# Kernel tuning notes

Hardware: AMD Instinct MI355X
Metric: run time of the kernel (lower is better)

Reference implementation:

```python
import jax, jax.numpy as jnp
import numpy as np

LEVEL_SHAPES = [(100, 134), (50, 67), (25, 34), (13, 17)]  # (H, W) per feature level
NH, NL, NP, D, DFF = 8, 4, 4, 256, 1024
DH = D // NH
LTOT = sum(h * w for h, w in LEVEL_SHAPES)  # 17821
BS, NQ = 4, 300


def _ln(x, w, b):
    m = x.mean(-1, keepdims=True)
    v = ((x - m) ** 2).mean(-1, keepdims=True)
    return (x - m) / jnp.sqrt(v + 1e-5) * w + b


def _mha(q, k, v, in_w, in_b, out_w, out_b):
    B, N, _ = q.shape
    wq, wk, wv = jnp.split(in_w, 3, axis=0)
    bq, bk, bv = jnp.split(in_b, 3)
    qh = (q @ wq.T + bq).reshape(B, N, NH, DH)
    kh = (k @ wk.T + bk).reshape(B, N, NH, DH)
    vh = (v @ wv.T + bv).reshape(B, N, NH, DH)
    a = jax.nn.softmax(jnp.einsum('bqhd,bkhd->bhqk', qh, kh) / float(np.sqrt(DH)), axis=-1)
    o = jnp.einsum('bhqk,bkhd->bqhd', a, vh).reshape(B, N, D)
    return o @ out_w.T + out_b


def _bilinear(img, grid):
    # img [B,C,H,W]; grid [B,N,2] in [-1,1]; align_corners=False, zero padding
    B, C, H, W = img.shape
    x = (grid[..., 0] + 1.0) * 0.5 * W - 0.5
    y = (grid[..., 1] + 1.0) * 0.5 * H - 0.5
    x0f = jnp.floor(x); y0f = jnp.floor(y)
    wx = x - x0f; wy = y - y0f
    x0 = x0f.astype(jnp.int32); y0 = y0f.astype(jnp.int32)
    flat = img.reshape(B, C, H * W)

    def gather(xi, yi):
        m = ((xi >= 0) & (xi < W) & (yi >= 0) & (yi < H)).astype(img.dtype)
        idx = jnp.clip(yi, 0, H - 1) * W + jnp.clip(xi, 0, W - 1)
        g = jnp.take_along_axis(flat, jnp.broadcast_to(idx[:, None, :], (B, C, idx.shape[-1])), axis=2)
        return g * m[:, None, :]

    return (gather(x0, y0) * ((1 - wx) * (1 - wy))[:, None]
            + gather(x0 + 1, y0) * (wx * (1 - wy))[:, None]
            + gather(x0, y0 + 1) * ((1 - wx) * wy)[:, None]
            + gather(x0 + 1, y0 + 1) * (wx * wy)[:, None])


def _msdeform(value, loc, aw):
    # value [B,L,NH,DH]; loc [B,Nq,NH,NL,NP,2] in [0,1]; aw [B,Nq,NH,NL,NP]
    B, Nq = loc.shape[0], loc.shape[1]
    outs = []
    start = 0
    for l, (Hl, Wl) in enumerate(LEVEL_SHAPES):
        v = value[:, start:start + Hl * Wl].transpose(0, 2, 3, 1).reshape(B * NH, DH, Hl, Wl)
        g = (2.0 * loc[:, :, :, l] - 1.0).transpose(0, 2, 1, 3, 4).reshape(B * NH, Nq * NP, 2)
        outs.append(_bilinear(v, g).reshape(B * NH, DH, Nq, NP))
        start += Hl * Wl
    samp = jnp.stack(outs, axis=3)  # [B*NH, DH, Nq, NL, NP]
    w = aw.transpose(0, 2, 1, 3, 4).reshape(B * NH, 1, Nq, NL, NP)
    out = (samp * w).sum(axis=(3, 4))  # [B*NH, DH, Nq]
    return out.reshape(B, NH, DH, Nq).transpose(0, 3, 1, 2).reshape(B, Nq, D)


def _deform_branch(q, ref, src_other, vw, vb, ow, ob, aww, awb, outw, outb):
    B, Nq, _ = q.shape
    value = (src_other @ vw.T + vb).reshape(B, -1, NH, DH)
    off = (q @ ow.T + ob).reshape(B, Nq, NH, NL, NP, 2)
    aw = jax.nn.softmax((q @ aww.T + awb).reshape(B, Nq, NH, NL * NP), axis=-1).reshape(B, Nq, NH, NL, NP)
    norm = jnp.array([[w, h] for h, w in LEVEL_SHAPES], dtype=q.dtype)  # (W,H) per level
    loc = ref[:, :, None, :, None, :] + off / norm[None, None, None, :, None, :]
    return _msdeform(value, loc, aw) @ outw.T + outb


def reference(tgt_RGB, tgt_T, query_pos_RGB, query_pos_T, ref_RGB, ref_T, src_RGB, src_T,
              sa_in_w, sa_in_b, sa_out_w, sa_out_b, ln_w, ln_b,
              ffn_w1, ffn_b1, ffn_w2, ffn_b2,
              val_w, val_b, off_w, off_b, aw_w, aw_b, cout_w, cout_b):
    # --- dual self-attention (eval mode: dropout = identity) ---
    q_RGB = tgt_RGB + query_pos_RGB
    q_T = tgt_T + query_pos_T
    sa_RGB = _mha(q_RGB, q_RGB, tgt_RGB, sa_in_w[0], sa_in_b[0], sa_out_w[0], sa_out_b[0])
    sa_T = _mha(q_T, q_T, tgt_T, sa_in_w[1], sa_in_b[1], sa_out_w[1], sa_out_b[1])
    tgt_RGB = _ln(tgt_RGB + sa_RGB, ln_w[0, 1], ln_b[0, 1])  # norm2_RGB
    tgt_T = _ln(tgt_T + sa_T, ln_w[1, 1], ln_b[1, 1])        # norm2_T
    # --- interactive multi-scale deformable cross-attn: RGB queries sample T memory & vice versa ---
    qc_RGB = tgt_RGB + query_pos_RGB
    qc_T = tgt_T + query_pos_T
    t2_RGB = _deform_branch(qc_RGB, ref_RGB, src_T, val_w[0], val_b[0], off_w[0], off_b[0], aw_w[0], aw_b[0], cout_w[0], cout_b[0])
    t2_T = _deform_branch(qc_T, ref_T, src_RGB, val_w[1], val_b[1], off_w[1], off_b[1], aw_w[1], aw_b[1], cout_w[1], cout_b[1])
    F_RGB, F_T = t2_RGB, t2_T
    # cross residuals exactly as in the torch layer (note the modality swap)
    r = tgt_T + t2_RGB
    t = r + t2_T
    tgt_RGB = _ln(r, ln_w[0, 0], ln_b[0, 0])  # norm1_RGB
    tgt_T = _ln(t, ln_w[1, 0], ln_b[1, 0])    # norm1_T
    # --- FFNs ---
    tgt_RGB = _ln(tgt_RGB + (jax.nn.relu(tgt_RGB @ ffn_w1[0].T + ffn_b1[0]) @ ffn_w2[0].T + ffn_b2[0]), ln_w[0, 2], ln_b[0, 2])
    tgt_T = _ln(tgt_T + (jax.nn.relu(tgt_T @ ffn_w1[1].T + ffn_b1[1]) @ ffn_w2[1].T + ffn_b2[1]), ln_w[1, 2], ln_b[1, 2])
    return tgt_RGB, tgt_T, F_RGB, F_T


def setup_inputs() -> dict:
    key = jax.random.key(0)
    ks = jax.random.split(key, 24)
    s = 0.05
    w = lambda k, shp: jax.random.normal(k, shp, dtype=jnp.float32) * s
    return {
        'tgt_RGB': jax.random.normal(ks[0], (BS, NQ, D), jnp.float32),
        'tgt_T': jax.random.normal(ks[1], (BS, NQ, D), jnp.float32),
        'query_pos_RGB': jax.random.normal(ks[2], (BS, NQ, D), jnp.float32),
        'query_pos_T': jax.random.normal(ks[3], (BS, NQ, D), jnp.float32),
        'ref_RGB': jax.random.uniform(ks[4], (BS, NQ, NL, 2), jnp.float32),
        'ref_T': jax.random.uniform(ks[5], (BS, NQ, NL, 2), jnp.float32),
        'src_RGB': jax.random.normal(ks[6], (BS, LTOT, D), jnp.float32),
        'src_T': jax.random.normal(ks[7], (BS, LTOT, D), jnp.float32),
        'sa_in_w': w(ks[8], (2, 3 * D, D)),
        'sa_in_b': jnp.zeros((2, 3 * D), jnp.float32),
        'sa_out_w': w(ks[9], (2, D, D)),
        'sa_out_b': jnp.zeros((2, D), jnp.float32),
        'ln_w': jnp.ones((2, 3, D), jnp.float32),
        'ln_b': jnp.zeros((2, 3, D), jnp.float32),
        'ffn_w1': w(ks[10], (2, DFF, D)),
        'ffn_b1': jnp.zeros((2, DFF), jnp.float32),
        'ffn_w2': w(ks[11], (2, D, DFF)),
        'ffn_b2': jnp.zeros((2, D), jnp.float32),
        'val_w': w(ks[12], (2, D, D)),
        'val_b': jnp.zeros((2, D), jnp.float32),
        'off_w': w(ks[13], (2, NH * NL * NP * 2, D)),
        'off_b': jax.random.normal(ks[14], (2, NH * NL * NP * 2), jnp.float32) * 0.5,
        'aw_w': w(ks[15], (2, NH * NL * NP, D)),
        'aw_b': jnp.zeros((2, NH * NL * NP), jnp.float32),
        'cout_w': w(ks[16], (2, D, D)),
        'cout_b': jnp.zeros((2, D), jnp.float32),
    }
```

## Files before the change

### kernel.cpp

```cpp
#include <hip/hip_runtime.h>
#include <hip/hip_bf16.h>
#include <cstddef>
#include <math.h>

#define NTOK 1200
#define LTOT_C 17821
#define MVAL 71284
#define STOK (NTOK * 256)

typedef __attribute__((ext_vector_type(8))) short bhalf8;
typedef __attribute__((ext_vector_type(4))) float f32x4;

static __device__ __forceinline__ short f2bf(float f) {
    unsigned u = __builtin_bit_cast(unsigned, f);
    u += 0x7fffu + ((u >> 16) & 1u);
    return (short)(u >> 16);
}
static __device__ __forceinline__ float bf2f(short s) {
    unsigned u = ((unsigned)(unsigned short)s) << 16;
    return __builtin_bit_cast(float, u);
}
static __device__ __forceinline__ bhalf8 cvt8(float4 a, float4 b) {
    bhalf8 h;
    h[0] = f2bf(a.x); h[1] = f2bf(a.y); h[2] = f2bf(a.z); h[3] = f2bf(a.w);
    h[4] = f2bf(b.x); h[5] = f2bf(b.y); h[6] = f2bf(b.z); h[7] = f2bf(b.w);
    return h;
}
static __device__ __forceinline__ void gload_lds16(const void* g, void* l) {
    __builtin_amdgcn_global_load_lds(
        (const __attribute__((address_space(1))) void*)g,
        (__attribute__((address_space(3))) void*)l, 16, 0, 0);
}

struct WcvtArgs { const float* s[10]; short* d[10]; int n[10]; };
__global__ __launch_bounds__(256) void wcvt(WcvtArgs a) {
    const int ti = blockIdx.y;
    const float* s = a.s[ti];
    short* d = a.d[ti];
    const int n = a.n[ti];
    for (int base = (blockIdx.x * 256 + threadIdx.x) * 8; base < n; base += gridDim.x * 256 * 8) {
        const float4 f0 = *reinterpret_cast<const float4*>(s + base);
        const float4 f1 = *reinterpret_cast<const float4*>(s + base + 4);
        *reinterpret_cast<bhalf8*>(d + base) = cvt8(f0, f1);
    }
}

__global__ __launch_bounds__(256) void prep_act(
    const float* __restrict__ tgt0, const float* __restrict__ tgt1,
    const float* __restrict__ pos0, const float* __restrict__ pos1,
    short* __restrict__ qb_bf, short* __restrict__ tgtb,
    const float* __restrict__ off_b, const float* __restrict__ aw_b,
    float* __restrict__ baw)
{
    const int z = blockIdx.y;
    if (blockIdx.x == 0 && z == 0) {
        for (int i = threadIdx.x; i < 768; i += 256) {
            const int zz = i / 384, j = i - zz * 384;
            baw[i] = (j < 256) ? off_b[zz * 256 + j] : aw_b[zz * 128 + (j - 256)];
        }
    }
    const float* tg = z ? tgt1 : tgt0;
    const float* ps = z ? pos1 : pos0;
    const int base = (blockIdx.x * 256 + threadIdx.x) * 8;
    if (base >= STOK) return;
    const float4 t0 = *reinterpret_cast<const float4*>(tg + base);
    const float4 t1 = *reinterpret_cast<const float4*>(tg + base + 4);
    const float4 p0 = *reinterpret_cast<const float4*>(ps + base);
    const float4 p1 = *reinterpret_cast<const float4*>(ps + base + 4);
    float4 s0 = make_float4(t0.x + p0.x, t0.y + p0.y, t0.z + p0.z, t0.w + p0.w);
    float4 s1 = make_float4(t1.x + p1.x, t1.y + p1.y, t1.z + p1.z, t1.w + p1.w);
    *reinterpret_cast<bhalf8*>(qb_bf + (size_t)z * STOK + base) = cvt8(s0, s1);
    *reinterpret_cast<bhalf8*>(tgtb + (size_t)z * STOK + base) = cvt8(t0, t1);
}

__global__ __launch_bounds__(256) void gemm_val(
    const float* __restrict__ A0, const float* __restrict__ A1,
    const short* __restrict__ Wbf, const float* __restrict__ bias,
    short* __restrict__ C)
{
    __shared__ alignas(16) short As[2][64 * 64];
    __shared__ alignas(16) short Bs[2][128 * 64];
    const int i = blockIdx.x;
    const int widx = (i & 7) * 557 + (i >> 3);
    const int x = widx & 1;
    const int yz = widx >> 1;
    const int z = yz / 1114;
    const int y = yz - z * 1114;
    const float* A = z ? A1 : A0;
    const short* W = Wbf + (size_t)z * 65536;
    const float* bz = bias + z * 256;
    short* Cz = C + (size_t)z * MVAL * 256;
    const int t = threadIdx.x;
    const int wave = t >> 6, lane = t & 63;
    const int l15 = lane & 15, l4 = lane >> 4;
    const int wr = wave >> 1, wc = wave & 1;
    const int bm = y * 64, bn = x * 128;
    f32x4 acc[2][4] = {};

    const int nr8 = lane >> 3, q8 = lane & 7;
    auto stageW = [&](int k0, int buf) {
        #pragma unroll
        for (int ii = 0; ii < 4; ++ii) {
            const int c = wave * 4 + ii;
            const int n = c * 8 + nr8;
            gload_lds16(W + (size_t)(bn + n) * 256 + k0 + ((q8 ^ nr8) << 3),
                        (char*)&Bs[buf][0] + c * 1024);
        }
    };
    float4 paf[2][2];
    auto issueA = [&](int k0) {
        #pragma unroll
        for (int ii = 0; ii < 2; ++ii) {
            const int G = t + ii * 256;
            const int m = G >> 3, g = G & 7;
            const int row = min(bm + m, MVAL - 1);
            const float* s = A + (size_t)row * 256 + k0 + g * 8;
            paf[ii][0] = *reinterpret_cast<const float4*>(s);
            paf[ii][1] = *reinterpret_cast<const float4*>(s + 4);
        }
    };
    auto commitA = [&](int buf) {
        #pragma unroll
        for (int ii = 0; ii < 2; ++ii) {
            const int G = t + ii * 256;
            const int m = G >> 3, g = G & 7;
            *reinterpret_cast<bhalf8*>(&As[buf][m * 64 + ((g ^ (m & 7)) << 3)]) =
                cvt8(paf[ii][0], paf[ii][1]);
        }
    };
    auto compute = [&](int buf) {
        #pragma unroll
        for (int kf = 0; kf < 2; ++kf) {
            bhalf8 af[2], bfv[4];
            #pragma unroll
            for (int mf = 0; mf < 2; ++mf) {
                const int m = wr * 32 + (mf << 4) + l15;
                const int g = ((kf << 2) + l4) ^ (m & 7);
                af[mf] = *reinterpret_cast<const bhalf8*>(&As[buf][m * 64 + (g << 3)]);
            }
            #pragma unroll
            for (int nf = 0; nf < 4; ++nf) {
                const int n = (wc << 6) + (nf << 4) + l15;
                const int g = ((kf << 2) + l4) ^ (n & 7);
                bfv[nf] = *reinterpret_cast<const bhalf8*>(&Bs[buf][n * 64 + (g << 3)]);
            }
            #pragma unroll
            for (int mf = 0; mf < 2; ++mf)
                #pragma unroll
                for (int nf = 0; nf < 4; ++nf)
                    acc[mf][nf] = __builtin_amdgcn_mfma_f32_16x16x32_bf16(
                        af[mf], bfv[nf], acc[mf][nf], 0, 0, 0);
        }
    };

    issueA(0);
    stageW(0, 0);
    commitA(0);
    __syncthreads();
    #pragma unroll
    for (int ks = 0; ks < 4; ++ks) {
        const int cur = ks & 1, nxt = cur ^ 1;
        if (ks + 1 < 4) {
            issueA((ks + 1) << 6);
            stageW((ks + 1) << 6, nxt);
        }
        compute(cur);
        if (ks + 1 < 4) commitA(nxt);
        __syncthreads();
    }

    float br[4];
    #pragma unroll
    for (int nf = 0; nf < 4; ++nf) br[nf] = bz[bn + (wc << 6) + (nf << 4) + l15];
    #pragma unroll
    for (int mf = 0; mf < 2; ++mf) {
        #pragma unroll
        for (int j = 0; j < 4; ++j) {
            const int row = bm + wr * 32 + (mf << 4) + (l4 << 2) + j;
            if (row >= MVAL) continue;
            const int colbase = bn + (wc << 6);
            #pragma unroll
            for (int nf = 0; nf < 4; ++nf)
                Cz[(size_t)row * 256 + colbase + (nf << 4) + l15] = f2bf(acc[mf][nf][j] + br[nf]);
        }
    }
}

template<bool HASRES, bool RELU, bool OUT_BF16, int BM, int NK>
__global__ __launch_bounds__(256) void gemm_bf16(
    const short* __restrict__ Av, size_t aStrideZ, int lda,
    const short* __restrict__ Wv, size_t wStrideZ, int ldw,
    const float* __restrict__ bias, size_t biasStrideZ,
    const float* __restrict__ Res0, const float* __restrict__ Res1, int ldr,
    void* __restrict__ Cv, size_t cStrideZ, int ldc,
    int M)
{
    constexpr int MFR = BM / 32;
    constexpr int ACW = BM / 32;
    __shared__ alignas(16) short As[2][BM * 64];
    __shared__ alignas(16) short Bs[2][128 * 64];
    const int z = blockIdx.z;
    const short* W = Wv + (size_t)z * wStrideZ;
    const float* bz = bias + (size_t)z * biasStrideZ;
    const int t = threadIdx.x;
    const int wave = t >> 6, lane = t & 63;
    const int l15 = lane & 15, l4 = lane >> 4;
    const int wr = wave >> 1, wc = wave & 1;
    const int bm = blockIdx.y * BM, bn = blockIdx.x * 128;
    f32x4 acc[MFR][4] = {};

    const int nr8 = lane >> 3, q8 = lane & 7;
    auto stageW = [&](int k0, int buf) {
        #pragma unroll
        for (int i = 0; i < 4; ++i) {
            const int c = wave * 4 + i;
            const int n = c * 8 + nr8;
            gload_lds16(W + (size_t)(bn + n) * ldw + k0 + ((q8 ^ nr8) << 3),
                        (char*)&Bs[buf][0] + c * 1024);
        }
    };
    auto stageA = [&](int k0, int buf) {
        #pragma unroll
        for (int i = 0; i < ACW; ++i) {
            const int c = wave * ACW + i;
            const int m = c * 8 + nr8;
            const int row = min(bm + m, M - 1);
            gload_lds16(Av + (size_t)z * aStrideZ + (size_t)row * lda + k0 + ((q8 ^ (m & 7)) << 3),
                        (char*)&As[buf][0] + c * 1024);
        }
    };
    auto compute = [&](int buf) {
        #pragma unroll
        for (int kf = 0; kf < 2; ++kf) {
            bhalf8 af[MFR], bfv[4];
            #pragma unroll
            for (int mf = 0; mf < MFR; ++mf) {
                const int m = wr * (BM / 2) + (mf << 4) + l15;
                const int g = ((kf << 2) + l4) ^ (m & 7);
                af[mf] = *reinterpret_cast<const bhalf8*>(&As[buf][m * 64 + (g << 3)]);
            }
            #pragma unroll
            for (int nf = 0; nf < 4; ++nf) {
                const int n = (wc << 6) + (nf << 4) + l15;
                const int g = ((kf << 2) + l4) ^ (n & 7);
                bfv[nf] = *reinterpret_cast<const bhalf8*>(&Bs[buf][n * 64 + (g << 3)]);
            }
            #pragma unroll
            for (int mf = 0; mf < MFR; ++mf)
                #pragma unroll
                for (int nf = 0; nf < 4; ++nf)
                    acc[mf][nf] = __builtin_amdgcn_mfma_f32_16x16x32_bf16(
                        af[mf], bfv[nf], acc[mf][nf], 0, 0, 0);
        }
    };

    stageA(0, 0);
    stageW(0, 0);
    __syncthreads();
    #pragma unroll
    for (int ks = 0; ks < NK; ++ks) {
        const int cur = ks & 1, nxt = cur ^ 1;
        if (ks + 1 < NK) {
            stageA((ks + 1) << 6, nxt);
            stageW((ks + 1) << 6, nxt);
        }
        compute(cur);
        __syncthreads();
    }

    const float* Rz = HASRES ? (z ? Res1 : Res0) : nullptr;
    float br[4];
    #pragma unroll
    for (int nf = 0; nf < 4; ++nf) br[nf] = bz[bn + (wc << 6) + (nf << 4) + l15];
    #pragma unroll
    for (int mf = 0; mf < MFR; ++mf) {
        #pragma unroll
        for (int j = 0; j < 4; ++j) {
            const int row = bm + wr * (BM / 2) + (mf << 4) + (l4 << 2) + j;
            if (row >= M) continue;
            const int colbase = bn + (wc << 6);
            #pragma unroll
            for (int nf = 0; nf < 4; ++nf) {
                const int col = colbase + (nf << 4) + l15;
                float v = acc[mf][nf][j] + br[nf];
                if (HASRES) v += Rz[(size_t)row * ldr + col];
                if (RELU) v = fmaxf(v, 0.f);
                if (OUT_BF16)
                    ((short*)Cv + (size_t)z * cStrideZ)[(size_t)row * ldc + col] = f2bf(v);
                else
                    ((float*)Cv + (size_t)z * cStrideZ)[(size_t)row * ldc + col] = v;
            }
        }
    }
}

__global__ __launch_bounds__(256) void attn2_kernel(
    const float* __restrict__ qkv_base, short* __restrict__ out_base)
{
    const float scale = 0.17677669529663687f;
    const float* qkv = qkv_base + (size_t)blockIdx.z * 921600;
    short* outp = out_base + (size_t)blockIdx.z * STOK;
    const int b = blockIdx.y >> 3, h = blockIdx.y & 7;
    const int t = threadIdx.x;
    const int ql = t & 31;
    const int kg = t >> 5;
    const int q = blockIdx.x * 32 + ql;
    const bool act = q < 300;
    const float* base = qkv + (size_t)b * 300 * 768;

    float qreg[32];
    if (act) {
        const float4* qp = reinterpret_cast<const float4*>(base + (size_t)q * 768 + h * 32);
        #pragma unroll
        for (int d4 = 0; d4 < 8; ++d4) {
            const float4 v = qp[d4];
            qreg[d4 * 4 + 0] = v.x; qreg[d4 * 4 + 1] = v.y;
            qreg[d4 * 4 + 2] = v.z; qreg[d4 * 4 + 3] = v.w;
        }
    }
    __shared__ float Ks[64][32];
    __shared__ float Vs[64][32];
    float m = -1e30f, l = 0.f, o[32];
    #pragma unroll
    for (int d = 0; d < 32; ++d) o[d] = 0.f;

    for (int k0 = 0; k0 < 300; k0 += 64) {
        const int cnt = min(64, 300 - k0);
        __syncthreads();
        for (int i = t; i < cnt * 32; i += 256) {
            const int kr = i >> 5, d = i & 31;
            Ks[kr][d] = base[(size_t)(k0 + kr) * 768 + 256 + h * 32 + d];
            Vs[kr][d] = base[(size_t)(k0 + kr) * 768 + 512 + h * 32 + d];
        }
        __syncthreads();
        if (act) {
            for (int kk = kg; kk < cnt; kk += 8) {
                const float4* krow = reinterpret_cast<const float4*>(&Ks[kk][0]);
                float s = 0.f;
                #pragma unroll
                for (int d4 = 0; d4 < 8; ++d4) {
                    const float4 kv = krow[d4];
                    s += qreg[d4 * 4 + 0] * kv.x + qreg[d4 * 4 + 1] * kv.y
                       + qreg[d4 * 4 + 2] * kv.z + qreg[d4 * 4 + 3] * kv.w;
                }
                s *= scale;
                const float4* vrow = reinterpret_cast<const float4*>(&Vs[kk][0]);
                if (s <= m) {
                    const float e = __expf(s - m);
                    l += e;
                    #pragma unroll
                    for (int d4 = 0; d4 < 8; ++d4) {
                        const float4 vv = vrow[d4];
                        o[d4 * 4 + 0] += e * vv.x; o[d4 * 4 + 1] += e * vv.y;
                        o[d4 * 4 + 2] += e * vv.z; o[d4 * 4 + 3] += e * vv.w;
                    }
                } else {
                    const float c = __expf(m - s);
                    l = l * c + 1.f;
                    #pragma unroll
                    for (int d4 = 0; d4 < 8; ++d4) {
                        const float4 vv = vrow[d4];
                        o[d4 * 4 + 0] = o[d4 * 4 + 0] * c + vv.x;
                        o[d4 * 4 + 1] = o[d4 * 4 + 1] * c + vv.y;
                        o[d4 * 4 + 2] = o[d4 * 4 + 2] * c + vv.z;
                        o[d4 * 4 + 3] = o[d4 * 4 + 3] * c + vv.w;
                    }
                    m = s;
                }
            }
        }
    }
    __shared__ float pm[32][8];
    __shared__ float pl[32][8];
    __shared__ float po[8][32][33];
    pm[ql][kg] = m; pl[ql][kg] = l;
    #pragma unroll
    for (int d = 0; d < 32; ++d) po[kg][d][ql] = o[d];
    __syncthreads();
    if (kg == 0) {
        float M = pm[ql][0];
        #pragma unroll
        for (int i = 1; i < 8; ++i) M = fmaxf(M, pm[ql][i]);
        float L = 0.f;
        #pragma unroll
        for (int i = 0; i < 8; ++i) L += pl[ql][i] * __expf(pm[ql][i] - M);
        const float invL = 1.f / L;
        #pragma unroll
        for (int i = 0; i < 8; ++i) pm[ql][i] = __expf(pm[ql][i] - M) * invL;
    }
    __syncthreads();
    if (act) {
        #pragma unroll
        for (int dd = 0; dd < 4; ++dd) {
            const int d = kg * 4 + dd;
            float v = 0.f;
            #pragma unroll
            for (int i = 0; i < 8; ++i) v += pm[ql][i] * po[i][d][ql];
            outp[((size_t)b * 300 + q) * 256 + h * 32 + d] = f2bf(v);
        }
    }
}

#define LN_BODY(vexpr, widx)                                                  \
    const int row = blockIdx.x, t = threadIdx.x, z = blockIdx.y;              \
    (void)z;                                                                  \
    const int i = row * 256 + t;                                              \
    const float v = (vexpr);                                                  \
    __shared__ float r1[4], r2[4];                                            \
    float s = v;                                                              \
    _Pragma("unroll")                                                         \
    for (int o = 32; o; o >>= 1) s += __shfl_xor(s, o);                       \
    if ((t & 63) == 0) r1[t >> 6] = s;                                        \
    __syncthreads();                                                          \
    const float mean = (r1[0] + r1[1] + r1[2] + r1[3]) * (1.f / 256.f);       \
    const float dd = v - mean;                                                \
    float sq = dd * dd;                                                       \
    _Pragma("unroll")                                                         \
    for (int o = 32; o; o >>= 1) sq += __shfl_xor(sq, o);                     \
    if ((t & 63) == 0) r2[t >> 6] = sq;                                       \
    __syncthreads();                                                          \
    const float var = (r2[0] + r2[1] + r2[2] + r2[3]) * (1.f / 256.f);        \
    const float y = dd * rsqrtf(var + 1e-5f) * ln_w[(widx) * 256 + t]         \
                    + ln_b[(widx) * 256 + t];

__global__ __launch_bounds__(256) void ln2_fused(
    const float* __restrict__ presum, const float* __restrict__ pos0,
    const float* __restrict__ pos1, const float* __restrict__ ln_w,
    const float* __restrict__ ln_b, short* __restrict__ qc_bf,
    float* __restrict__ tgt2T)
{
    LN_BODY(presum[(size_t)z * STOK + i], z * 3 + 1)
    const float* pos = z ? pos1 : pos0;
    qc_bf[(size_t)z * STOK + i] = f2bf(y + pos[i]);
    if (z == 1) tgt2T[i] = y;
}

__global__ __launch_bounds__(256) void ln1_fused(
    const float* __restrict__ tgt2T, const float* __restrict__ out2,
    const float* __restrict__ out3, const float* __restrict__ ln_w,
    const float* __restrict__ ln_b, short* __restrict__ ln1b,
    float* __restrict__ ln1f)
{
    LN_BODY(tgt2T[row * 256 + t] + out2[row * 256 + t] + (z ? out3[row * 256 + t] : 0.f), z * 3 + 0)
    ln1b[(size_t)z * STOK + i] = f2bf(y);
    ln1f[(size_t)z * STOK + i] = y;
}

__global__ __launch_bounds__(256) void ln3_kernel(
    const float* __restrict__ ffny, const float* __restrict__ ln_w,
    const float* __restrict__ ln_b, float* __restrict__ o0,
    float* __restrict__ o1)
{
    LN_BODY(ffny[(size_t)z * STOK + i], z * 3 + 2)
    (z ? o1 : o0)[i] = y;
}

__global__ __launch_bounds__(256) void sample_kernel(
    const short* __restrict__ valb, const float* __restrict__ oaw,
    const float* __restrict__ ref0, const float* __restrict__ ref1,
    short* __restrict__ out)
{
    const int HL[4] = {100, 50, 25, 13};
    const int WL[4] = {134, 67, 34, 17};
    const int ST[4] = {0, 13400, 16750, 17600};
    const int z = blockIdx.y;
    const int t = threadIdx.x;
    const int wave = t >> 6, lane = t & 63;
    const int qi = wave >> 1, hh = wave & 1;
    const int pp = lane >> 5, h4 = (lane >> 3) & 3, dl = lane & 7;
    const int h = hh * 4 + h4;
    const int bq = blockIdx.x * 2 + qi;
    const int b = bq / 300;
    const float* op = oaw + ((size_t)z * NTOK + bq) * 384;
    const float* offp = op + h * 32;
    const float* awp  = op + 256 + h * 16;
    const float* refp = (z ? ref1 : ref0) + (size_t)bq * 8;
    const short* vb = valb + (size_t)z * MVAL * 256 + (size_t)b * LTOT_C * 256;
    const int co = h * 32 + dl * 4;

    float w16[16];
    float mx = -1e30f;
    #pragma unroll
    for (int i = 0; i < 16; ++i) { w16[i] = awp[i]; mx = fmaxf(mx, w16[i]); }
    float ssum = 0.f;
    #pragma unroll
    for (int i = 0; i < 16; ++i) { w16[i] = __expf(w16[i] - mx); ssum += w16[i]; }
    const float sinv = 1.f / ssum;

    float a0 = 0.f, a1 = 0.f, a2 = 0.f, a3 = 0.f;
#define TAP(cond, ridx, wv)                                                   \
    if (cond) {                                                               \
        const short4 sv = *reinterpret_cast<const short4*>(                   \
            vb + (size_t)(ridx) * 256 + co);                                  \
        a0 += (wv) * bf2f(sv.x); a1 += (wv) * bf2f(sv.y);                     \
        a2 += (wv) * bf2f(sv.z); a3 += (wv) * bf2f(sv.w);                     \
    }
    #pragma unroll
    for (int l = 0; l < 4; ++l) {
        const int Wl = WL[l], Hl = HL[l];
        const float rx = refp[l * 2] * (float)Wl - 0.5f;
        const float ry = refp[l * 2 + 1] * (float)Hl - 0.5f;
        #pragma unroll
        for (int j = 0; j < 2; ++j) {
            const int p = pp * 2 + j;
            const float px = rx + offp[(l * 4 + p) * 2];
            const float py = ry + offp[(l * 4 + p) * 2 + 1];
            const float wgt = w16[l * 4 + p] * sinv;
            const float x0f = floorf(px), y0f = floorf(py);
            const float wx = px - x0f, wy = py - y0f;
            const int x0 = (int)x0f, y0 = (int)y0f;
            const bool xa = (x0 >= 0) & (x0 < Wl);
            const bool xb = (x0 >= -1) & (x0 < Wl - 1);
            const bool ya = (y0 >= 0) & (y0 < Hl);
            const bool yb = (y0 >= -1) & (y0 < Hl - 1);
            const int rbase = ST[l] + y0 * Wl + x0;
            const float w00 = wgt * (1.f - wx) * (1.f - wy);
            const float w10 = wgt * wx * (1.f - wy);
            const float w01 = wgt * (1.f - wx) * wy;
            const float w11 = wgt * wx * wy;
            TAP(ya & xa, rbase, w00)
            TAP(ya & xb, rbase + 1, w10)
            TAP(yb & xa, rbase + Wl, w01)
            TAP(yb & xb, rbase + Wl + 1, w11)
        }
    }
#undef TAP
    a0 += __shfl_xor(a0, 32);
    a1 += __shfl_xor(a1, 32);
    a2 += __shfl_xor(a2, 32);
    a3 += __shfl_xor(a3, 32);
    if (pp == 0) {
        short4 o;
        o.x = f2bf(a0); o.y = f2bf(a1); o.z = f2bf(a2); o.w = f2bf(a3);
        *reinterpret_cast<short4*>(&out[((size_t)z * NTOK + bq) * 256 + co]) = o;
    }
}

extern "C" void kernel_launch(void* const* d_in, const int* in_sizes, int n_in,
                              void* d_out, int out_size, void* d_ws, size_t ws_size,
                              hipStream_t stream) {
    const float* tgt[2] = {(const float*)d_in[0], (const float*)d_in[1]};
    const float* pos[2] = {(const float*)d_in[2], (const float*)d_in[3]};
    const float* ref[2] = {(const float*)d_in[4], (const float*)d_in[5]};
    const float* src[2] = {(const float*)d_in[6], (const float*)d_in[7]};
    const float* sa_in_w  = (const float*)d_in[8];
    const float* sa_in_b  = (const float*)d_in[9];
    const float* sa_out_w = (const float*)d_in[10];
    const float* sa_out_b = (const float*)d_in[11];
    const float* ln_w = (const float*)d_in[12];
    const float* ln_b = (const float*)d_in[13];
    const float* ffn_w1 = (const float*)d_in[14];
    const float* ffn_b1 = (const float*)d_in[15];
    const float* ffn_w2 = (const float*)d_in[16];
    const float* ffn_b2 = (const float*)d_in[17];
    const float* val_w = (const float*)d_in[18];
    const float* val_b = (const float*)d_in[19];
    const float* off_w = (const float*)d_in[20];
    const float* off_b = (const float*)d_in[21];
    const float* aw_w = (const float*)d_in[22];
    const float* aw_b = (const float*)d_in[23];
    const float* cout_w = (const float*)d_in[24];
    const float* cout_b = (const float*)d_in[25];

    char* base = (char*)d_ws;
    size_t off = 0;
    auto alloc = [&](size_t bytes) -> char* {
        char* p = base + off;
        off += (bytes + 255) & ~(size_t)255;
        return p;
    };
    short* wbf   = (short*)alloc((size_t)2031616 * 2);
    float* baw   = (float*)alloc(768 * 4);
    short* qb_bf = (short*)alloc((size_t)2 * STOK * 2);
    short* tgtb  = (short*)alloc((size_t)2 * STOK * 2);
    float* qkv   = (float*)alloc((size_t)2 * 921600 * 4);
    short* attno = (short*)alloc((size_t)2 * STOK * 2);
    float* presum= (float*)alloc((size_t)2 * STOK * 4);
    short* qc_bf = (short*)alloc((size_t)2 * STOK * 2);
    float* tgt2T = (float*)alloc((size_t)STOK * 4);
    float* oawb  = (float*)alloc((size_t)2 * NTOK * 384 * 4);
    short* valb  = (short*)alloc((size_t)2 * MVAL * 256 * 2);
    short* samp  = (short*)alloc((size_t)2 * STOK * 2);
    short* ln1b  = (short*)alloc((size_t)2 * STOK * 2);
    float* ln1f  = (float*)alloc((size_t)2 * STOK * 4);
    short* ffnh  = (short*)alloc((size_t)2 * NTOK * 1024 * 2);
    float* ffny  = (float*)alloc((size_t)2 * STOK * 4);

    short* sa_in_bf  = wbf + 0;
    short* sa_out_bf = wbf + 393216;
    short* ffn1_bf   = wbf + 524288;
    short* ffn2_bf   = wbf + 1048576;
    short* val_bf    = wbf + 1572864;
    short* cout_bf   = wbf + 1703936;
    short* oaw_bf    = wbf + 1835008;

    float* out0 = (float*)d_out;
    float* out1 = out0 + STOK;
    float* out2 = out1 + STOK;
    float* out3 = out2 + STOK;

    const dim3 b256(256);

    WcvtArgs wa;
    wa.s[0] = sa_in_w;        wa.d[0] = sa_in_bf;       wa.n[0] = 393216;
    wa.s[1] = sa_out_w;       wa.d[1] = sa_out_bf;      wa.n[1] = 131072;
    wa.s[2] = ffn_w1;         wa.d[2] = ffn1_bf;        wa.n[2] = 524288;
    wa.s[3] = ffn_w2;         wa.d[3] = ffn2_bf;        wa.n[3] = 524288;
    wa.s[4] = val_w;          wa.d[4] = val_bf;         wa.n[4] = 131072;
    wa.s[5] = cout_w;         wa.d[5] = cout_bf;        wa.n[5] = 131072;
    wa.s[6] = off_w;          wa.d[6] = oaw_bf;         wa.n[6] = 65536;
    wa.s[7] = aw_w;           wa.d[7] = oaw_bf + 65536; wa.n[7] = 32768;
    wa.s[8] = off_w + 65536;  wa.d[8] = oaw_bf + 98304; wa.n[8] = 65536;
    wa.s[9] = aw_w + 32768;   wa.d[9] = oaw_bf + 163840;wa.n[9] = 32768;
    wcvt<<<dim3(128, 10), b256, 0, stream>>>(wa);

    prep_act<<<dim3(150, 2), b256, 0, stream>>>(tgt[0], tgt[1], pos[0], pos[1],
                                                qb_bf, tgtb, off_b, aw_b, baw);

    gemm_val<<<dim3(4456), b256, 0, stream>>>(src[1], src[0], val_bf, val_b, valb);

    gemm_bf16<false, false, false, 64, 4><<<dim3(4, 19, 2), b256, 0, stream>>>(
        qb_bf, (size_t)STOK, 256, sa_in_bf, 196608, 256, sa_in_b, 768,
        nullptr, nullptr, 0, qkv, 921600, 768, NTOK);
    gemm_bf16<false, false, false, 64, 4><<<dim3(2, 19, 2), b256, 0, stream>>>(
        tgtb, (size_t)STOK, 256, sa_in_bf + 512 * 256, 196608, 256, sa_in_b + 512, 768,
        nullptr, nullptr, 0, qkv + 512, 921600, 768, NTOK);

    attn2_kernel<<<dim3(10, 32, 2), b256, 0, stream>>>(qkv, attno);

    gemm_bf16<true, false, false, 64, 4><<<dim3(2, 19, 2), b256, 0, stream>>>(
        attno, (size_t)STOK, 256, sa_out_bf, 65536, 256, sa_out_b, 256,
        tgt[0], tgt[1], 256, presum, (size_t)STOK, 256, NTOK);

    ln2_fused<<<dim3(NTOK, 2), b256, 0, stream>>>(presum, pos[0], pos[1], ln_w, ln_b, qc_bf, tgt2T);

    gemm_bf16<false, false, false, 64, 4><<<dim3(3, 19, 2), b256, 0, stream>>>(
        qc_bf, (size_t)STOK, 256, oaw_bf, 98304, 256, baw, 384,
        nullptr, nullptr, 0, oawb, (size_t)NTOK * 384, 384, NTOK);

    sample_kernel<<<dim3(600, 2), b256, 0, stream>>>(valb, oawb, ref[0], ref[1], samp);

    gemm_bf16<false, false, false, 64, 4><<<dim3(2, 19, 2), b256, 0, stream>>>(
        samp, (size_t)STOK, 256, cout_bf, 65536, 256, cout_b, 256,
        nullptr, nullptr, 0, out2, (size_t)STOK, 256, NTOK);

    ln1_fused<<<dim3(NTOK, 2), b256, 0, stream>>>(tgt2T, out2, out3, ln_w, ln_b, ln1b, ln1f);

    gemm_bf16<false, true, true, 64, 4><<<dim3(8, 19, 2), b256, 0, stream>>>(
        ln1b, (size_t)STOK, 256, ffn1_bf, 262144, 256, ffn_b1, 1024,
        nullptr, nullptr, 0, ffnh, (size_t)NTOK * 1024, 1024, NTOK);

    gemm_bf16<true, false, false, 64, 16><<<dim3(2, 19, 2), b256, 0, stream>>>(
        ffnh, (size_t)NTOK * 1024, 1024, ffn2_bf, 262144, 1024, ffn_b2, 256,
        ln1f, ln1f + STOK, 256, ffny, (size_t)STOK, 256, NTOK);

    ln3_kernel<<<dim3(NTOK, 2), b256, 0, stream>>>(ffny, ln_w, ln_b, out0, out1);
}
```

Measured before the change: 199.5 us.

## Deepen gemm_val A-prefetch to two stages and merge QK/V projection launches

The value-projection GEMM now holds two register slots of fp32 A tiles in flight. The K loop is unrolled by hand, with explicit vmcnt/lgkmcnt waits and raw barriers, so global loads for step k+2 overlap compute on step k. Separately, the generic bf16 GEMM takes a second A pointer chosen by blockIdx.x, which lets the QK and V input projections run as one launch. This is meant to hide global-load latency in the largest GEMM and remove one kernel launch, at the cost of more registers and hand-tuned wait counts that are fragile.

After: 191.0 us. 1.04x faster.

```diff
diff --git a/kernel.cpp b/kernel.cpp
--- a/kernel.cpp
+++ b/kernel.cpp
@@ -31,6 +31,12 @@
         (const __attribute__((address_space(1))) void*)g,
         (__attribute__((address_space(3))) void*)l, 16, 0, 0);
 }
+#define WAIT_LGKM0_BAR() do { \
+    asm volatile("s_waitcnt lgkmcnt(0)" ::: "memory"); \
+    __builtin_amdgcn_sched_barrier(0); \
+    __builtin_amdgcn_s_barrier(); \
+    __builtin_amdgcn_sched_barrier(0); \
+} while (0)
 
 struct WcvtArgs { const float* s[10]; short* d[10]; int n[10]; };
 __global__ __launch_bounds__(256) void wcvt(WcvtArgs a) {
@@ -107,25 +113,25 @@
                         (char*)&Bs[buf][0] + c * 1024);
         }
     };
-    float4 paf[2][2];
-    auto issueA = [&](int k0) {
+    float4 paf[2][2][2];
+    auto issueA = [&](int k0, int slot) {
         #pragma unroll
         for (int ii = 0; ii < 2; ++ii) {
             const int G = t + ii * 256;
             const int m = G >> 3, g = G & 7;
             const int row = min(bm + m, MVAL - 1);
             const float* s = A + (size_t)row * 256 + k0 + g * 8;
-            paf[ii][0] = *reinterpret_cast<const float4*>(s);
-            paf[ii][1] = *reinterpret_cast<const float4*>(s + 4);
-        }
-    };
-    auto commitA = [&](int buf) {
+            paf[slot][ii][0] = *reinterpret_cast<const float4*>(s);
+            paf[slot][ii][1] = *reinterpret_cast<const float4*>(s + 4);
+        }
+    };
+    auto commitA = [&](int slot, int buf) {
         #pragma unroll
         for (int ii = 0; ii < 2; ++ii) {
             const int G = t + ii * 256;
             const int m = G >> 3, g = G & 7;
             *reinterpret_cast<bhalf8*>(&As[buf][m * 64 + ((g ^ (m & 7)) << 3)]) =
-                cvt8(paf[ii][0], paf[ii][1]);
+                cvt8(paf[slot][ii][0], paf[slot][ii][1]);
         }
     };
     auto compute = [&](int buf) {
@@ -153,21 +159,37 @@
         }
     };
 
-    issueA(0);
-    stageW(0, 0);
-    commitA(0);
-    __syncthreads();
-    #pragma unroll
-    for (int ks = 0; ks < 4; ++ks) {
-        const int cur = ks & 1, nxt = cur ^ 1;
-        if (ks + 1 < 4) {
-            issueA((ks + 1) << 6);
-            stageW((ks + 1) << 6, nxt);
-        }
-        compute(cur);
-        if (ks + 1 < 4) commitA(nxt);
-        __syncthreads();
-    }
+    issueA(0, 0);   stageW(0, 0);
+    issueA(64, 1);  stageW(64, 1);
+    asm volatile("s_waitcnt vmcnt(8)" ::: "memory");
+    __builtin_amdgcn_sched_barrier(0);
+    commitA(0, 0);
+    WAIT_LGKM0_BAR();
+
+    compute(0);
+    WAIT_LGKM0_BAR();
+    issueA(128, 0); stageW(128, 0);
+    asm volatile("s_waitcnt vmcnt(8)" ::: "memory");
+    __builtin_amdgcn_sched_barrier(0);
+    commitA(1, 1);
+    WAIT_LGKM0_BAR();
+
+    compute(1);
+    WAIT_LGKM0_BAR();
+    issueA(192, 1); stageW(192, 1);
+    asm volatile("s_waitcnt vmcnt(8)" ::: "memory");
+    __builtin_amdgcn_sched_barrier(0);
+    commitA(0, 0);
+    WAIT_LGKM0_BAR();
+
+    compute(0);
+    WAIT_LGKM0_BAR();
+    asm volatile("s_waitcnt vmcnt(0)" ::: "memory");
+    __builtin_amdgcn_sched_barrier(0);
+    commitA(1, 1);
+    WAIT_LGKM0_BAR();
+
+    compute(1);
 
     float br[4];
     #pragma unroll
@@ -188,7 +210,8 @@
 
 template<bool HASRES, bool RELU, bool OUT_BF16, int BM, int NK>
 __global__ __launch_bounds__(256) void gemm_bf16(
-    const short* __restrict__ Av, size_t aStrideZ, int lda,
+    const short* __restrict__ Av, const short* __restrict__ Av2, int xsplit,
+    size_t aStrideZ, int lda,
     const short* __restrict__ Wv, size_t wStrideZ, int ldw,
     const float* __restrict__ bias, size_t biasStrideZ,
     const float* __restrict__ Res0, const float* __restrict__ Res1, int ldr,
@@ -200,6 +223,7 @@
     __shared__ alignas(16) short As[2][BM * 64];
     __shared__ alignas(16) short Bs[2][128 * 64];
     const int z = blockIdx.z;
+    const short* Abase = (Av2 != nullptr && (int)blockIdx.x >= xsplit) ? Av2 : Av;
     const short* W = Wv + (size_t)z * wStrideZ;
     const float* bz = bias + (size_t)z * biasStrideZ;
     const int t = threadIdx.x;
@@ -225,7 +249,7 @@
             const int c = wave * ACW + i;
             const int m = c * 8 + nr8;
             const int row = min(bm + m, M - 1);
-            gload_lds16(Av + (size_t)z * aStrideZ + (size_t)row * lda + k0 + ((q8 ^ (m & 7)) << 3),
+            gload_lds16(Abase + (size_t)z * aStrideZ + (size_t)row * lda + k0 + ((q8 ^ (m & 7)) << 3),
                         (char*)&As[buf][0] + c * 1024);
         }
     };
@@ -619,39 +643,36 @@
 
     gemm_val<<<dim3(4456), b256, 0, stream>>>(src[1], src[0], val_bf, val_b, valb);
 
-    gemm_bf16<false, false, false, 64, 4><<<dim3(4, 19, 2), b256, 0, stream>>>(
-        qb_bf, (size_t)STOK, 256, sa_in_bf, 196608, 256, sa_in_b, 768,
+    gemm_bf16<false, false, false, 64, 4><<<dim3(6, 19, 2), b256, 0, stream>>>(
+        qb_bf, tgtb, 4, (size_t)STOK, 256, sa_in_bf, 196608, 256, sa_in_b, 768,
         nullptr, nullptr, 0, qkv, 921600, 768, NTOK);
+
+    attn2_kernel<<<dim3(10, 32, 2), b256, 0, stream>>>(qkv, attno);
+
+    gemm_bf16<true, false, false, 64, 4><<<dim3(2, 19, 2), b256, 0, stream>>>(
+        attno, nullptr, 1 << 30, (size_t)STOK, 256, sa_out_bf, 65536, 256, sa_out_b, 256,
+        tgt[0], tgt[1], 256, presum, (size_t)STOK, 256, NTOK);
+
+    ln2_fused<<<dim3(NTOK, 2), b256, 0, stream>>>(presum, pos[0], pos[1], ln_w, ln_b, qc_bf, tgt2T);
+
+    gemm_bf16<false, false, false, 64, 4><<<dim3(3, 19, 2), b256, 0, stream>>>(
+        qc_bf, nullptr, 1 << 30, (size_t)STOK, 256, oaw_bf, 98304, 256, baw, 384,
+        nullptr, nullptr, 0, oawb, (size_t)NTOK * 384, 384, NTOK);
+
+    sample_kernel<<<dim3(600, 2), b256, 0, stream>>>(valb, oawb, ref[0], ref[1], samp);
+
     gemm_bf16<false, false, false, 64, 4><<<dim3(2, 19, 2), b256, 0, stream>>>(
-        tgtb, (size_t)STOK, 256, sa_in_bf + 512 * 256, 196608, 256, sa_in_b + 512, 768,
-        nullptr, nullptr, 0, qkv + 512, 921600, 768, NTOK);
-
-    attn2_kernel<<<dim3(10, 32, 2), b256, 0, stream>>>(qkv, attno);
-
-    gemm_bf16<true, false, false, 64, 4><<<dim3(2, 19, 2), b256, 0, stream>>>(
-        attno, (size_t)STOK, 256, sa_out_bf, 65536, 256, sa_out_b, 256,
-        tgt[0], tgt[1], 256, presum, (size_t)STOK, 256, NTOK);
-
-    ln2_fused<<<dim3(NTOK, 2), b256, 0, stream>>>(presum, pos[0], pos[1], ln_w, ln_b, qc_bf, tgt2T);
-
-    gemm_bf16<false, false, false, 64, 4><<<dim3(3, 19, 2), b256, 0, stream>>>(
-        qc_bf, (size_t)STOK, 256, oaw_bf, 98304, 256, baw, 384,
-        nullptr, nullptr, 0, oawb, (size_t)NTOK * 384, 384, NTOK);
-
-    sample_kernel<<<dim3(600, 2), b256, 0, stream>>>(valb, oawb, ref[0], ref[1], samp);
-
-    gemm_bf16<false, false, false, 64, 4><<<dim3(2, 19, 2), b256, 0, stream>>>(
-        samp, (size_t)STOK, 256, cout_bf, 65536, 256, cout_b, 256,
+        samp, nullptr, 1 << 30, (size_t)STOK, 256, cout_bf, 65536, 256, cout_b, 256,
         nullptr, nullptr, 0, out2, (size_t)STOK, 256, NTOK);
 
     ln1_fused<<<dim3(NTOK, 2), b256, 0, stream>>>(tgt2T, out2, out3, ln_w, ln_b, ln1b, ln1f);
 
     gemm_bf16<false, true, true, 64, 4><<<dim3(8, 19, 2), b256, 0, stream>>>(
-        ln1b, (size_t)STOK, 256, ffn1_bf, 262144, 256, ffn_b1, 1024,
+        ln1b, nullptr, 1 << 30, (size_t)STOK, 256, ffn1_bf, 262144, 256, ffn_b1, 1024,
         nullptr, nullptr, 0, ffnh, (size_t)NTOK * 1024, 1024, NTOK);
 
     gemm_bf16<true, false, false, 64, 16><<<dim3(2, 19, 2), b256, 0, stream>>>(
-        ffnh, (size_t)NTOK * 1024, 1024, ffn2_bf, 262144, 1024, ffn_b2, 256,
+        ffnh, nullptr, 1 << 30, (size_t)NTOK * 1024, 1024, ffn2_bf, 262144, 1024, ffn_b2, 256,
         ln1f, ln1f + STOK, 256, ffny, (size_t)STOK, 256, NTOK);
 
     ln3_kernel<<<dim3(NTOK, 2), b256, 0, stream>>>(ffny, ln_w, ln_b, out0, out1);
```
